# Kernel tuning notes

Hardware: AMD Instinct MI355X
Metric: run time of the kernel (lower is better)

Reference implementation:

```python
import jax, jax.numpy as jnp
import numpy as np

B, N, Q, K = 8, 1024, 128, 16  # batch, surface points, query points, d_embedding


def _layer_norm(x, w, b, eps=1e-5):
    m = x.mean(-1, keepdims=True)
    v = ((x - m) ** 2).mean(-1, keepdims=True)
    return (x - m) * jax.lax.rsqrt(v + eps) * w + b


def _positional_embedding(coords, pe_log_scale, k):
    # coords: [..., 2] -> [..., k]; layout [sin(x/d_i), cos(x/d_i), sin(y/d_i), cos(y/d_i)]
    num = k // 4
    div = jnp.exp(pe_log_scale) ** (4.0 * jnp.arange(num, dtype=jnp.float32) / k)  # [num]
    x = coords[..., 0:1] / div  # [..., num]
    y = coords[..., 1:2] / div
    pe = jnp.stack([jnp.sin(x), jnp.cos(x), jnp.sin(y), jnp.cos(y)], axis=-1)  # [..., num, 4]
    return pe.reshape(coords.shape[:-1] + (k,))


def setup_inputs() -> dict:
    key = jax.random.key(0)
    ks = jax.random.split(key, 8)
    return {
        'lm_s': jax.random.normal(ks[0], (B, N), jnp.float32),
        'ttm_s': jax.random.uniform(ks[1], (B, N), jnp.float32),
        'tv_s': jax.random.uniform(ks[2], (B, N), jnp.float32) + 0.05,
        'lm_q': jax.random.normal(ks[3], (B, Q), jnp.float32),
        'ttm_q': jax.random.uniform(ks[4], (B, Q), jnp.float32),
        # learned params
        'log_scale_kernels': 0.1 * jax.random.normal(ks[5], (K, 2), jnp.float32),  # per-kernel elliptical log scales
        'ln_s_w': jnp.ones((K,), jnp.float32),
        'ln_s_b': jnp.zeros((K,), jnp.float32),
        'ln_q_w': jnp.ones((K,), jnp.float32),
        'ln_q_b': jnp.zeros((K,), jnp.float32),
        'pe_log_scale': jnp.log(jnp.float32(10000.0)),
    }


def reference(lm_s, ttm_s, tv_s, lm_q, ttm_q,
              log_scale_kernels, ln_s_w, ln_s_b, ln_q_w, ln_q_b, pe_log_scale):
    k = log_scale_kernels.shape[0]
    # bandwidth_i = erfinv(i/(K+1)) * sqrt(2), i = 1..K
    i = jnp.arange(1, k + 1, dtype=jnp.float32)
    bw = jax.scipy.special.erfinv(i / (k + 1)) * jnp.sqrt(jnp.float32(2.0))  # [K]

    coords_s = jnp.stack([lm_s, ttm_s], axis=-1)   # [B,N,2]
    coords_q = jnp.stack([lm_q, ttm_q], axis=-1)   # [B,Q,2]
    all_coords = jnp.concatenate([coords_s, coords_q], axis=1)  # [B,M,2], M=N+Q

    # pairwise squared differences to surface points
    diff2 = (all_coords[:, :, None, :] - coords_s[:, None, :, :]) ** 2  # [B,M,N,2]

    scale = jnp.exp(log_scale_kernels)        # [K,2]
    tr = scale.sum(-1)                         # [K]
    # normalized elliptical distances per kernel
    nd = jnp.einsum('bmnc,kc->bkmn', diff2, scale) / tr[None, :, None, None]
    kern = jnp.exp(-nd / (2.0 * bw ** 2)[None, :, None, None])  # [B,K,M,N]

    wsum = jnp.einsum('bkmn,bn->bmk', kern, tv_s)   # [B,M,K]
    norm = kern.sum(-1).transpose(0, 2, 1)          # [B,M,K]
    emb = wsum / norm                                # [B,M,K]

    n = coords_s.shape[1]
    surf_emb = _layer_norm(emb[:, :n], ln_s_w, ln_s_b)
    query_emb = _layer_norm(emb[:, n:], ln_q_w, ln_q_b)

    sqrt2 = jnp.sqrt(jnp.float32(2.0))
    surf_out = surf_emb + _positional_embedding(coords_s, pe_log_scale, k) * sqrt2
    query_out = query_emb + _positional_embedding(coords_q, pe_log_scale, k) * sqrt2
    return jnp.concatenate([surf_out, query_out], axis=1)  # [B,M,K]
```

## Files before the change

### kernel.cpp

```cpp
#include <hip/hip_runtime.h>
#include <math.h>

namespace {
constexpr int B = 8, N = 1024, Q = 128, K = 16, M = N + Q;
constexpr int WAVES_PER_BLOCK = 4;
constexpr int NWAVES = B * M;
constexpr int NBLOCKS = NWAVES / WAVES_PER_BLOCK;
}

#if __has_builtin(__builtin_amdgcn_exp2f)
  #define EXP2F(x) __builtin_amdgcn_exp2f(x)
#else
  #define EXP2F(x) exp2f(x)
#endif

__global__ void IvySPT_prep(const float* __restrict__ lsk, float* __restrict__ cc) {
  int k = threadIdx.x;
  if (k < K) {
    float s0 = expf(lsk[2 * k + 0]);
    float s1 = expf(lsk[2 * k + 1]);
    float tr = s0 + s1;
    float x  = (float)(k + 1) / (float)(K + 1);
    float bw = erfinvf(x) * 1.41421356237309504880f;
    float denom = tr * 2.0f * bw * bw;
    const float LOG2E = 1.44269504088896340736f;
    cc[k]     = -s0 * LOG2E / denom;
    cc[K + k] = -s1 * LOG2E / denom;
  }
}

__global__ __launch_bounds__(256) void IvySPT_main(
    const float* __restrict__ lm_s, const float* __restrict__ ttm_s,
    const float* __restrict__ tv_s, const float* __restrict__ lm_q,
    const float* __restrict__ ttm_q,
    const float* __restrict__ ln_s_w, const float* __restrict__ ln_s_b,
    const float* __restrict__ ln_q_w, const float* __restrict__ ln_q_b,
    const float* __restrict__ pls_p, const float* __restrict__ cc,
    float* __restrict__ out)
{
  const int lane = threadIdx.x & 63;
  const int wid  = threadIdx.x >> 6;
  const int w    = blockIdx.x * WAVES_PER_BLOCK + wid;
  const int b    = w / M;
  const int m    = w - b * M;

  float cmx, cmy;
  if (m < N) { cmx = lm_s[b * N + m];       cmy = ttm_s[b * N + m]; }
  else       { cmx = lm_q[b * Q + (m - N)]; cmy = ttm_q[b * Q + (m - N)]; }

  float cA[K], cB[K];
#pragma unroll
  for (int k = 0; k < K; k++) { cA[k] = cc[k]; cB[k] = cc[K + k]; }

  float wsum[K], nrm[K];
#pragma unroll
  for (int k = 0; k < K; k++) { wsum[k] = 0.f; nrm[k] = 0.f; }

  const float* xs = lm_s  + b * N;
  const float* ys = ttm_s + b * N;
  const float* tv = tv_s  + b * N;

#pragma unroll 4
  for (int i = 0; i < N / 64; i++) {
    const int n = lane + 64 * i;
    float sx = xs[n], sy = ys[n], t = tv[n];
    float dx = cmx - sx, dy = cmy - sy;
    float dx2 = dx * dx, dy2 = dy * dy;
#pragma unroll
    for (int k = 0; k < K; k++) {
      float e = EXP2F(fmaf(dy2, cB[k], dx2 * cA[k]));
      wsum[k] = fmaf(e, t, wsum[k]);
      nrm[k] += e;
    }
  }

  __shared__ float red[WAVES_PER_BLOCK][64][17];
  float (*rp)[17] = red[wid];
  const int col = lane & 15;
  const int qq  = lane >> 4;

  float totW, totN;
  {
#pragma unroll
    for (int c = 0; c < K; c++) rp[lane][c] = wsum[c];
    asm volatile("s_waitcnt lgkmcnt(0)" ::: "memory");
    float s = 0.f;
#pragma unroll
    for (int r = 0; r < 16; r++) s += rp[qq * 16 + r][col];
    asm volatile("s_waitcnt lgkmcnt(0)" ::: "memory");
    s += __shfl_xor(s, 16);
    s += __shfl_xor(s, 32);
    totW = s;
  }
  {
#pragma unroll
    for (int c = 0; c < K; c++) rp[lane][c] = nrm[c];
    asm volatile("s_waitcnt lgkmcnt(0)" ::: "memory");
    float s = 0.f;
#pragma unroll
    for (int r = 0; r < 16; r++) s += rp[qq * 16 + r][col];
    s += __shfl_xor(s, 16);
    s += __shfl_xor(s, 32);
    totN = s;
  }

  float emb = totW / totN;

  float s1 = emb;
  s1 += __shfl_xor(s1, 1); s1 += __shfl_xor(s1, 2);
  s1 += __shfl_xor(s1, 4); s1 += __shfl_xor(s1, 8);
  float mean = s1 * (1.f / 16.f);
  float dv = emb - mean;
  float s2 = dv * dv;
  s2 += __shfl_xor(s2, 1); s2 += __shfl_xor(s2, 2);
  s2 += __shfl_xor(s2, 4); s2 += __shfl_xor(s2, 8);
  float inv = rsqrtf(s2 * (1.f / 16.f) + 1e-5f);

  const int k = col;
  float lw, lb;
  if (m < N) { lw = ln_s_w[k]; lb = ln_s_b[k]; }
  else       { lw = ln_q_w[k]; lb = ln_q_b[k]; }
  float normed = dv * inv * lw + lb;

  float pls = pls_p[0];
  float invdiv = expf(-pls * (float)(k >> 2) * 0.25f);
  float cv  = (k & 2) ? cmy : cmx;
  float arg = cv * invdiv;
  float pe  = (k & 1) ? cosf(arg) : sinf(arg);
  float val = fmaf(pe, 1.41421356237309504880f, normed);

  if (lane < 16) out[((size_t)(b * M + m)) * K + k] = val;
}

extern "C" void kernel_launch(void* const* d_in, const int* in_sizes, int n_in,
                              void* d_out, int out_size, void* d_ws, size_t ws_size,
                              hipStream_t stream) {
  const float* lm_s   = (const float*)d_in[0];
  const float* ttm_s  = (const float*)d_in[1];
  const float* tv_s   = (const float*)d_in[2];
  const float* lm_q   = (const float*)d_in[3];
  const float* ttm_q  = (const float*)d_in[4];
  const float* lsk    = (const float*)d_in[5];
  const float* ln_s_w = (const float*)d_in[6];
  const float* ln_s_b = (const float*)d_in[7];
  const float* ln_q_w = (const float*)d_in[8];
  const float* ln_q_b = (const float*)d_in[9];
  const float* pls    = (const float*)d_in[10];

  float* cc  = (float*)d_ws;
  float* out = (float*)d_out;

  hipLaunchKernelGGL(IvySPT_prep, dim3(1), dim3(64), 0, stream, lsk, cc);
  hipLaunchKernelGGL(IvySPT_main, dim3(NBLOCKS), dim3(256), 0, stream,
                     lm_s, ttm_s, tv_s, lm_q, ttm_q,
                     ln_s_w, ln_s_b, ln_q_w, ln_q_b, pls, cc, out);
}
```

Measured before the change: 35.95 us.

## Fuse coefficient prep into main kernel and pack exponent arguments as float2

Removes the separate single-block prep launch and instead has each block compute the per-kernel exponent coefficients into shared memory, followed by a block barrier. The exponent argument computation is packed into two-wide float vectors so the compiler can emit packed FMA/multiply instructions, and the outer loop unroll drops from 4 to 2. This saves one kernel launch and its serialization, plus some VALU work, at the cost of redundant erfinv/exp work and a __syncthreads in every block.

After: 30.09 us. 1.19x faster.

```diff
diff --git a/kernel.cpp b/kernel.cpp
--- a/kernel.cpp
+++ b/kernel.cpp
@@ -6,6 +6,7 @@
 constexpr int WAVES_PER_BLOCK = 4;
 constexpr int NWAVES = B * M;
 constexpr int NBLOCKS = NWAVES / WAVES_PER_BLOCK;
+typedef float f32x2 __attribute__((ext_vector_type(2)));
 }
 
 #if __has_builtin(__builtin_amdgcn_exp2f)
@@ -14,9 +15,24 @@
   #define EXP2F(x) exp2f(x)
 #endif
 
-__global__ void IvySPT_prep(const float* __restrict__ lsk, float* __restrict__ cc) {
-  int k = threadIdx.x;
-  if (k < K) {
+#if __has_builtin(__builtin_elementwise_fma)
+  #define VFMA2(a, b, c) __builtin_elementwise_fma((a), (b), (c))
+#else
+  #define VFMA2(a, b, c) ((a) * (b) + (c))
+#endif
+
+__global__ __launch_bounds__(256) void IvySPT_main(
+    const float* __restrict__ lm_s, const float* __restrict__ ttm_s,
+    const float* __restrict__ tv_s, const float* __restrict__ lm_q,
+    const float* __restrict__ ttm_q, const float* __restrict__ lsk,
+    const float* __restrict__ ln_s_w, const float* __restrict__ ln_s_b,
+    const float* __restrict__ ln_q_w, const float* __restrict__ ln_q_b,
+    const float* __restrict__ pls_p,
+    float* __restrict__ out)
+{
+  __shared__ float sC[2][K];
+  if (threadIdx.x < K) {
+    const int k = threadIdx.x;
     float s0 = expf(lsk[2 * k + 0]);
     float s1 = expf(lsk[2 * k + 1]);
     float tr = s0 + s1;
@@ -24,20 +40,11 @@
     float bw = erfinvf(x) * 1.41421356237309504880f;
     float denom = tr * 2.0f * bw * bw;
     const float LOG2E = 1.44269504088896340736f;
-    cc[k]     = -s0 * LOG2E / denom;
-    cc[K + k] = -s1 * LOG2E / denom;
+    sC[0][k] = -s0 * LOG2E / denom;
+    sC[1][k] = -s1 * LOG2E / denom;
   }
-}
+  __syncthreads();
 
-__global__ __launch_bounds__(256) void IvySPT_main(
-    const float* __restrict__ lm_s, const float* __restrict__ ttm_s,
-    const float* __restrict__ tv_s, const float* __restrict__ lm_q,
-    const float* __restrict__ ttm_q,
-    const float* __restrict__ ln_s_w, const float* __restrict__ ln_s_b,
-    const float* __restrict__ ln_q_w, const float* __restrict__ ln_q_b,
-    const float* __restrict__ pls_p, const float* __restrict__ cc,
-    float* __restrict__ out)
-{
   const int lane = threadIdx.x & 63;
   const int wid  = threadIdx.x >> 6;
   const int w    = blockIdx.x * WAVES_PER_BLOCK + wid;
@@ -48,9 +55,12 @@
   if (m < N) { cmx = lm_s[b * N + m];       cmy = ttm_s[b * N + m]; }
   else       { cmx = lm_q[b * Q + (m - N)]; cmy = ttm_q[b * Q + (m - N)]; }
 
-  float cA[K], cB[K];
+  f32x2 cA2[K / 2], cB2[K / 2];
 #pragma unroll
-  for (int k = 0; k < K; k++) { cA[k] = cc[k]; cB[k] = cc[K + k]; }
+  for (int j = 0; j < K / 2; j++) {
+    cA2[j] = f32x2{sC[0][2 * j], sC[0][2 * j + 1]};
+    cB2[j] = f32x2{sC[1][2 * j], sC[1][2 * j + 1]};
+  }
 
   float wsum[K], nrm[K];
 #pragma unroll
@@ -60,17 +70,21 @@
   const float* ys = ttm_s + b * N;
   const float* tv = tv_s  + b * N;
 
-#pragma unroll 4
+#pragma unroll 2
   for (int i = 0; i < N / 64; i++) {
     const int n = lane + 64 * i;
     float sx = xs[n], sy = ys[n], t = tv[n];
     float dx = cmx - sx, dy = cmy - sy;
     float dx2 = dx * dx, dy2 = dy * dy;
+    f32x2 dx2v = {dx2, dx2};
+    f32x2 dy2v = {dy2, dy2};
 #pragma unroll
-    for (int k = 0; k < K; k++) {
-      float e = EXP2F(fmaf(dy2, cB[k], dx2 * cA[k]));
-      wsum[k] = fmaf(e, t, wsum[k]);
-      nrm[k] += e;
+    for (int j = 0; j < K / 2; j++) {
+      f32x2 arg = VFMA2(dy2v, cB2[j], dx2v * cA2[j]);
+      float e0 = EXP2F(arg.x);
+      float e1 = EXP2F(arg.y);
+      wsum[2 * j]     = fmaf(e0, t, wsum[2 * j]);     nrm[2 * j]     += e0;
+      wsum[2 * j + 1] = fmaf(e1, t, wsum[2 * j + 1]); nrm[2 * j + 1] += e1;
     }
   }
 
@@ -147,11 +161,9 @@
   const float* ln_q_b = (const float*)d_in[9];
   const float* pls    = (const float*)d_in[10];
 
-  float* cc  = (float*)d_ws;
   float* out = (float*)d_out;
 
-  hipLaunchKernelGGL(IvySPT_prep, dim3(1), dim3(64), 0, stream, lsk, cc);
   hipLaunchKernelGGL(IvySPT_main, dim3(NBLOCKS), dim3(256), 0, stream,
-                     lm_s, ttm_s, tv_s, lm_q, ttm_q,
-                     ln_s_w, ln_s_b, ln_q_w, ln_q_b, pls, cc, out);
+                     lm_s, ttm_s, tv_s, lm_q, ttm_q, lsk,
+                     ln_s_w, ln_s_b, ln_q_w, ln_q_b, pls, out);
 }
```
